# Performance work log

Hardware: AMD Instinct MI355X
Metric: run time of the kernel (lower is better)

The kernel has to match this reference:

```python
import jax, jax.numpy as jnp
import numpy as np


def setup_inputs() -> dict:
    key = jax.random.key(0)
    ks = jax.random.split(key, 6)
    B, T, D, H = 32, 2048, 1024, 1024
    s = jax.random.normal(ks[0], (1, B, D), dtype=jnp.float32)
    h = jax.random.normal(ks[1], (B, T, D), dtype=jnp.float32)
    mask = jax.random.randint(ks[2], (B, T), 0, 2, dtype=jnp.int32)
    W = jax.random.normal(ks[3], (D, H), dtype=jnp.float32) * (6.0 / (D + H)) ** 0.5
    U = jax.random.normal(ks[4], (D, H), dtype=jnp.float32) * (6.0 / (D + H)) ** 0.5
    v = jax.random.normal(ks[5], (H, 1), dtype=jnp.float32) * (6.0 / (H + 1)) ** 0.5
    return {"s": s, "h": h, "mask": mask, "W": W, "U": U, "v": v}


def reference(s, h, mask, W, U, v):
    # mask-fill encoder states: zero out padded timesteps
    m = (mask != 0)[:, :, None]            # (B, T, 1)
    h = jnp.where(m, h, 0.0)               # (B, T, D)
    s_t = jnp.transpose(s, (1, 0, 2))      # (B, 1, D)
    proj_s = s_t @ W                       # (B, 1, H)
    proj_h = h @ U                         # (B, T, H)
    energy = jnp.tanh(proj_s + proj_h) @ v  # (B, T, 1)
    energy = jnp.where(m, energy, -1e9)
    score = jax.nn.softmax(energy, axis=1)  # softmax over time
    context = jnp.sum(score * h, axis=1)    # (B, D)
    return context
```

## Files before the change

### kernel.cpp

```cpp
#include <hip/hip_runtime.h>
#include <hip/hip_fp16.h>
#include <math.h>

#define BB 32
#define TT 2048
#define DD 1024
#define HH 1024
#define MM (BB*TT)

typedef _Float16 half8 __attribute__((ext_vector_type(8)));
typedef float f32x4 __attribute__((ext_vector_type(4)));

__device__ __forceinline__ float tanh_fast(float x) {
    float cx = fminf(fmaxf(x, -10.0f), 10.0f);
    float e2 = __expf(2.0f * cx);
    return (e2 - 1.0f) / (e2 + 1.0f);
}

__device__ __forceinline__ void load_lds16(const _Float16* g, _Float16* l) {
    __builtin_amdgcn_global_load_lds(
        (const __attribute__((address_space(1))) void*)g,
        (__attribute__((address_space(3))) void*)l, 16, 0, 0);
}

__global__ void compact_kernel(const int* __restrict__ mask,
                               int* __restrict__ rowlist,
                               int* __restrict__ cnts) {
    const int b = blockIdx.x, tid = threadIdx.x;
    const int lane = tid & 63, w = tid >> 6;
    const int* mb = mask + b * TT;
    const int t0 = tid * 8;
    int m[8], c = 0;
#pragma unroll
    for (int j = 0; j < 8; ++j) { m[j] = (mb[t0 + j] != 0); c += m[j]; }
    int pref = c;
#pragma unroll
    for (int off = 1; off < 64; off <<= 1) {
        int nv = __shfl_up(pref, off, 64);
        if (lane >= off) pref += nv;
    }
    __shared__ int wsum[4];
    if (lane == 63) wsum[w] = pref;
    __syncthreads();
    int wbase = 0;
    for (int i = 0; i < w; ++i) wbase += wsum[i];
    int pos = wbase + pref - c;
#pragma unroll
    for (int j = 0; j < 8; ++j)
        if (m[j]) rowlist[b * TT + pos++] = t0 + j;
    const int total = wsum[0] + wsum[1] + wsum[2] + wsum[3];
    if (tid == 0) cnts[b] = total;
    __syncthreads();
    const int padded = ((total + 127) >> 7) << 7;
    const int lastt = (total > 0) ? rowlist[b * TT + total - 1] : 0;
    for (int ci = total + tid; ci < padded; ci += 256)
        rowlist[b * TT + ci] = lastt;
}

__global__ void tiles_kernel(const int* __restrict__ cnts,
                             int* __restrict__ tile_b,
                             int* __restrict__ tile_ci,
                             int* __restrict__ ntiles) {
    if (threadIdx.x == 0) {
        int tot = 0;
        for (int b = 0; b < BB; ++b) {
            const int nt = (cnts[b] + 127) >> 7;
            for (int i = 0; i < nt; ++i) { tile_b[tot] = b; tile_ci[tot] = i * 128; ++tot; }
        }
        *ntiles = tot;
    }
}

__global__ void cast_h_kernel(const float* __restrict__ h,
                              const int* __restrict__ mask,
                              _Float16* __restrict__ h16) {
    const int row = blockIdx.x * 2 + (threadIdx.x >> 7);
    if (mask[row] == 0) return;
    const int c = (threadIdx.x & 127) * 8;
    const long base = (long)row * DD + c;
    const float4 f0 = *(const float4*)(h + base);
    const float4 f1 = *(const float4*)(h + base + 4);
    half8 o;
    o[0] = (_Float16)f0.x; o[1] = (_Float16)f0.y;
    o[2] = (_Float16)f0.z; o[3] = (_Float16)f0.w;
    o[4] = (_Float16)f1.x; o[5] = (_Float16)f1.y;
    o[6] = (_Float16)f1.z; o[7] = (_Float16)f1.w;
    *(half8*)(h16 + base) = o;
}

__global__ void prep_ut_kernel(const float* __restrict__ U,
                               _Float16* __restrict__ Ut) {
    __shared__ float tile[32][33];
    const int bx = blockIdx.x, by = blockIdx.y;
    const int tx = threadIdx.x & 31, ty = threadIdx.x >> 5;
#pragma unroll
    for (int j = 0; j < 4; ++j)
        tile[ty + j * 8][tx] = U[(long)(by * 32 + ty + j * 8) * HH + bx * 32 + tx];
    __syncthreads();
#pragma unroll
    for (int j = 0; j < 4; ++j)
        Ut[(long)(bx * 32 + ty + j * 8) * DD + by * 32 + tx] =
            (_Float16)tile[tx][ty + j * 8];
}

__global__ void prep_ps_kernel(const float* __restrict__ s,
                               const float* __restrict__ W,
                               float* __restrict__ ps,
                               float* __restrict__ out) {
    const int b = blockIdx.x, nseg = blockIdx.y;
    const int n = nseg * 256 + threadIdx.x;
    __shared__ float ss[DD];
#pragma unroll
    for (int j = 0; j < 4; ++j)
        ss[threadIdx.x + j * 256] = s[b * DD + threadIdx.x + j * 256];
    out[b * DD + n] = 0.0f;
    __syncthreads();
    float a[8];
#pragma unroll
    for (int j = 0; j < 8; ++j) a[j] = 0.f;
    for (int d = 0; d < DD; d += 8) {
#pragma unroll
        for (int j = 0; j < 8; ++j)
            a[j] += ss[d + j] * W[(long)(d + j) * HH + n];
    }
    ps[b * HH + n] = ((a[0]+a[1])+(a[2]+a[3])) + ((a[4]+a[5])+(a[6]+a[7]));
}

#define Bb_K 32

__global__ __launch_bounds__(256)
void energy_gemm_kernel(const _Float16* __restrict__ h16,
                        const _Float16* __restrict__ Ut,
                        const float* __restrict__ ps,
                        const float* __restrict__ v,
                        const int* __restrict__ rowlist,
                        const int* __restrict__ tile_b,
                        const int* __restrict__ tile_ci,
                        const int* __restrict__ ntiles,
                        float* __restrict__ epart) {
    const int mt = blockIdx.y;
    if (mt >= *ntiles) return;
    __shared__ _Float16 As[128][32];
    __shared__ _Float16 Bs[128][32];
    __shared__ float ps_s[128];
    __shared__ float v_s[128];
    __shared__ int   rl[128];

    const int nt = blockIdx.x;
    const int b   = tile_b[mt];
    const int ci0 = tile_ci[mt];
    const int n0  = nt * 128;
    const int tid = threadIdx.x;
    const int wave = tid >> 6, lane = tid & 63;
    const int wm = wave >> 1, wn = wave & 1;

    if (tid < 128) {
        ps_s[tid] = ps[b * HH + n0 + tid];
        v_s[tid]  = v[n0 + tid];
        rl[tid]   = rowlist[b * TT + ci0 + tid];
    }
    __syncthreads();

    const int srow = wave * 32 + (lane >> 2);
    const int sseg = (lane & 3) * 8;
    const _Float16* gA0 = h16 + ((long)b * TT + rl[srow])      * DD + sseg;
    const _Float16* gA1 = h16 + ((long)b * TT + rl[srow + 16]) * DD + sseg;
    const _Float16* gB0 = Ut + (long)(n0 + srow) * DD + sseg;
    const _Float16* gB1 = gB0 + 16 * DD;
    _Float16* lA0 = &As[wave * 32][0];
    _Float16* lA1 = &As[wave * 32 + 16][0];
    _Float16* lB0 = &Bs[wave * 32][0];
    _Float16* lB1 = &Bs[wave * 32 + 16][0];

    f32x4 acc[4][4];
#pragma unroll
    for (int i = 0; i < 4; ++i)
#pragma unroll
        for (int j = 0; j < 4; ++j) acc[i][j] = (f32x4)0.0f;

    const int lk = (lane >> 4) * 8;
    const int lr = lane & 15;

#pragma unroll 1
    for (int k0 = 0; k0 < DD; k0 += Bb_K) {
        __syncthreads();
        load_lds16(gA0 + k0, lA0);
        load_lds16(gA1 + k0, lA1);
        load_lds16(gB0 + k0, lB0);
        load_lds16(gB1 + k0, lB1);
        __syncthreads();

        half8 af[4], bf[4];
#pragma unroll
        for (int tm = 0; tm < 4; ++tm)
            af[tm] = *(const half8*)&As[wm * 64 + tm * 16 + lr][lk];
#pragma unroll
        for (int tn = 0; tn < 4; ++tn)
            bf[tn] = *(const half8*)&Bs[wn * 64 + tn * 16 + lr][lk];
#pragma unroll
        for (int tm = 0; tm < 4; ++tm)
#pragma unroll
            for (int tn = 0; tn < 4; ++tn)
                acc[tm][tn] = __builtin_amdgcn_mfma_f32_16x16x32_f16(
                    af[tm], bf[tn], acc[tm][tn], 0, 0, 0);
    }

    float part[4][4];
#pragma unroll
    for (int tm = 0; tm < 4; ++tm) {
#pragma unroll
        for (int r = 0; r < 4; ++r) {
            float p = 0.f;
#pragma unroll
            for (int tn = 0; tn < 4; ++tn) {
                const int cl = wn * 64 + tn * 16 + lr;
                p += v_s[cl] * tanh_fast(acc[tm][tn][r] + ps_s[cl]);
            }
            part[tm][r] = p;
        }
    }
#pragma unroll
    for (int off = 1; off < 16; off <<= 1)
#pragma unroll
        for (int tm = 0; tm < 4; ++tm)
#pragma unroll
            for (int r = 0; r < 4; ++r)
                part[tm][r] += __shfl_xor(part[tm][r], off, 64);

    if ((lane & 15) == 0) {
        const int slot = nt * 2 + wn;
#pragma unroll
        for (int tm = 0; tm < 4; ++tm)
#pragma unroll
            for (int r = 0; r < 4; ++r) {
                const int ci = ci0 + wm * 64 + tm * 16 + (lane >> 4) * 4 + r;
                epart[(long)slot * MM + b * TT + ci] = part[tm][r];
            }
    }
}

__global__ void softmax_kernel(const float* __restrict__ epart,
                               const int* __restrict__ rowlist,
                               const int* __restrict__ cnts,
                               float* __restrict__ score) {
    const int b = blockIdx.x, tid = threadIdx.x;
    const int cnt = cnts[b];
    for (int t = tid; t < TT; t += 256) score[b * TT + t] = 0.0f;

    float e[8], mx = -1e30f;
#pragma unroll
    for (int i = 0; i < 8; ++i) {
        const int ci = i * 256 + tid;
        float sum = -1e30f;
        if (ci < cnt) {
            sum = 0.f;
#pragma unroll
            for (int p = 0; p < 16; ++p)
                sum += epart[(long)p * MM + b * TT + ci];
        }
        e[i] = sum;
        mx = fmaxf(mx, sum);
    }
#pragma unroll
    for (int off = 32; off > 0; off >>= 1) mx = fmaxf(mx, __shfl_xor(mx, off, 64));
    __shared__ float r4[4];
    if ((tid & 63) == 0) r4[tid >> 6] = mx;
    __syncthreads();
    mx = fmaxf(fmaxf(r4[0], r4[1]), fmaxf(r4[2], r4[3]));

    float tot = 0.f;
#pragma unroll
    for (int i = 0; i < 8; ++i) {
        const int ci = i * 256 + tid;
        e[i] = (ci < cnt) ? __expf(e[i] - mx) : 0.0f;
        tot += e[i];
    }
#pragma unroll
    for (int off = 32; off > 0; off >>= 1) tot += __shfl_xor(tot, off, 64);
    __shared__ float s4[4];
    if ((tid & 63) == 0) s4[tid >> 6] = tot;
    __syncthreads();
    tot = s4[0] + s4[1] + s4[2] + s4[3];
    const float inv = 1.0f / tot;
#pragma unroll
    for (int i = 0; i < 8; ++i) {
        const int ci = i * 256 + tid;
        if (ci < cnt)
            score[b * TT + rowlist[b * TT + ci]] = e[i] * inv;
    }
}

__global__ void context_kernel(const _Float16* __restrict__ h16,
                               const float* __restrict__ score,
                               float* __restrict__ out) {
    const int tc = blockIdx.x;
    const int b  = blockIdx.y;
    const int d0 = threadIdx.x * 8;
    float a[8];
#pragma unroll
    for (int j = 0; j < 8; ++j) a[j] = 0.f;
    for (int i = 0; i < 128; ++i) {
        const int t = tc * 128 + i;
        const float sc = score[(long)b * TT + t];
        if (sc != 0.0f) {
            const half8 hv = *(const half8*)(h16 + ((long)(b * TT + t)) * DD + d0);
#pragma unroll
            for (int j = 0; j < 8; ++j) a[j] += sc * (float)hv[j];
        }
    }
#pragma unroll
    for (int j = 0; j < 8; ++j) atomicAdd(&out[b * DD + d0 + j], a[j]);
}

extern "C" void kernel_launch(void* const* d_in, const int* in_sizes, int n_in,
                              void* d_out, int out_size, void* d_ws, size_t ws_size,
                              hipStream_t stream) {
    const float* s    = (const float*)d_in[0];
    const float* h    = (const float*)d_in[1];
    const int*   mask = (const int*)  d_in[2];
    const float* W    = (const float*)d_in[3];
    const float* U    = (const float*)d_in[4];
    const float* v    = (const float*)d_in[5];
    float* out = (float*)d_out;

    char* ws = (char*)d_ws;
    size_t off = 0;
    _Float16* h16 = (_Float16*)(ws + off); off += (size_t)MM * DD * 2;
    _Float16* Ut  = (_Float16*)(ws + off); off += (size_t)HH * DD * 2;
    float*    ps  = (float*)(ws + off);    off += (size_t)BB * HH * 4;
    float*    ep  = (float*)(ws + off);    off += (size_t)16 * MM * 4;
    float*    scr = (float*)(ws + off);    off += (size_t)MM * 4;
    int*      rlist = (int*)(ws + off);    off += (size_t)MM * 4;
    int*      cnts  = (int*)(ws + off);    off += 64 * 4;
    int*      tb    = (int*)(ws + off);    off += 512 * 4;
    int*      tci   = (int*)(ws + off);    off += 512 * 4;
    int*      ntl   = (int*)(ws + off);

    compact_kernel<<<BB, 256, 0, stream>>>(mask, rlist, cnts);
    tiles_kernel  <<<1, 64, 0, stream>>>(cnts, tb, tci, ntl);
    cast_h_kernel <<<MM / 2, 256, 0, stream>>>(h, mask, h16);
    prep_ut_kernel<<<dim3(32, 32), 256, 0, stream>>>(U, Ut);
    prep_ps_kernel<<<dim3(32, 4), 256, 0, stream>>>(s, W, ps, out);
    energy_gemm_kernel<<<dim3(8, 512), 256, 0, stream>>>(h16, Ut, ps, v,
                                                         rlist, tb, tci, ntl, ep);
    softmax_kernel<<<BB, 256, 0, stream>>>(ep, rlist, cnts, scr);
    context_kernel<<<dim3(16, 32), 128, 0, stream>>>(h16, scr, out);
}
```

Before: 559.7 us.

## Fuse setup kernels, drop tile list, swizzle LDS and raise MFMA priority

Merges the compaction, cast, U transpose and s·W projection kernels into one launch that dispatches on block index. The separate tile-list kernel goes away: each GEMM block derives its batch and row chunk from its index and exits early when past the valid count. The grid is reordered so the M-tile is the fast dimension, an XOR swizzle is applied to the LDS k-segment to reduce bank conflicts on fragment reads, and s_setprio is raised around the MFMA block. The GEMM now launches a fixed 512x8 grid with early-exit blocks, and the fused setup kernel shares one LDS allocation across its roles.

```diff
diff --git a/kernel.cpp b/kernel.cpp
--- a/kernel.cpp
+++ b/kernel.cpp
@@ -23,107 +23,113 @@
         (__attribute__((address_space(3))) void*)l, 16, 0, 0);
 }
 
-__global__ void compact_kernel(const int* __restrict__ mask,
-                               int* __restrict__ rowlist,
-                               int* __restrict__ cnts) {
-    const int b = blockIdx.x, tid = threadIdx.x;
-    const int lane = tid & 63, w = tid >> 6;
-    const int* mb = mask + b * TT;
-    const int t0 = tid * 8;
-    int m[8], c = 0;
-#pragma unroll
-    for (int j = 0; j < 8; ++j) { m[j] = (mb[t0 + j] != 0); c += m[j]; }
-    int pref = c;
-#pragma unroll
-    for (int off = 1; off < 64; off <<= 1) {
-        int nv = __shfl_up(pref, off, 64);
-        if (lane >= off) pref += nv;
-    }
+#define CAST_BLOCKS (MM/2)
+#define UT_BLOCKS   1024
+#define PS_BLOCKS   128
+#define CPT_BLOCKS  32
+#define TOTAL_SETUP (CAST_BLOCKS + UT_BLOCKS + PS_BLOCKS + CPT_BLOCKS)
+
+__global__ __launch_bounds__(256)
+void mega_setup_kernel(const float* __restrict__ h,
+                       const int* __restrict__ mask,
+                       _Float16* __restrict__ h16,
+                       const float* __restrict__ U,
+                       _Float16* __restrict__ Ut,
+                       const float* __restrict__ s,
+                       const float* __restrict__ W,
+                       float* __restrict__ ps,
+                       float* __restrict__ out,
+                       int* __restrict__ rowlist,
+                       int* __restrict__ cnts) {
+    __shared__ float smem[1056];
     __shared__ int wsum[4];
-    if (lane == 63) wsum[w] = pref;
-    __syncthreads();
-    int wbase = 0;
-    for (int i = 0; i < w; ++i) wbase += wsum[i];
-    int pos = wbase + pref - c;
-#pragma unroll
-    for (int j = 0; j < 8; ++j)
-        if (m[j]) rowlist[b * TT + pos++] = t0 + j;
-    const int total = wsum[0] + wsum[1] + wsum[2] + wsum[3];
-    if (tid == 0) cnts[b] = total;
-    __syncthreads();
-    const int padded = ((total + 127) >> 7) << 7;
-    const int lastt = (total > 0) ? rowlist[b * TT + total - 1] : 0;
-    for (int ci = total + tid; ci < padded; ci += 256)
-        rowlist[b * TT + ci] = lastt;
-}
-
-__global__ void tiles_kernel(const int* __restrict__ cnts,
-                             int* __restrict__ tile_b,
-                             int* __restrict__ tile_ci,
-                             int* __restrict__ ntiles) {
-    if (threadIdx.x == 0) {
-        int tot = 0;
-        for (int b = 0; b < BB; ++b) {
-            const int nt = (cnts[b] + 127) >> 7;
-            for (int i = 0; i < nt; ++i) { tile_b[tot] = b; tile_ci[tot] = i * 128; ++tot; }
-        }
-        *ntiles = tot;
-    }
-}
-
-__global__ void cast_h_kernel(const float* __restrict__ h,
-                              const int* __restrict__ mask,
-                              _Float16* __restrict__ h16) {
-    const int row = blockIdx.x * 2 + (threadIdx.x >> 7);
-    if (mask[row] == 0) return;
-    const int c = (threadIdx.x & 127) * 8;
-    const long base = (long)row * DD + c;
-    const float4 f0 = *(const float4*)(h + base);
-    const float4 f1 = *(const float4*)(h + base + 4);
-    half8 o;
-    o[0] = (_Float16)f0.x; o[1] = (_Float16)f0.y;
-    o[2] = (_Float16)f0.z; o[3] = (_Float16)f0.w;
-    o[4] = (_Float16)f1.x; o[5] = (_Float16)f1.y;
-    o[6] = (_Float16)f1.z; o[7] = (_Float16)f1.w;
-    *(half8*)(h16 + base) = o;
-}
-
-__global__ void prep_ut_kernel(const float* __restrict__ U,
-                               _Float16* __restrict__ Ut) {
-    __shared__ float tile[32][33];
-    const int bx = blockIdx.x, by = blockIdx.y;
-    const int tx = threadIdx.x & 31, ty = threadIdx.x >> 5;
-#pragma unroll
-    for (int j = 0; j < 4; ++j)
-        tile[ty + j * 8][tx] = U[(long)(by * 32 + ty + j * 8) * HH + bx * 32 + tx];
-    __syncthreads();
-#pragma unroll
-    for (int j = 0; j < 4; ++j)
-        Ut[(long)(bx * 32 + ty + j * 8) * DD + by * 32 + tx] =
-            (_Float16)tile[tx][ty + j * 8];
-}
-
-__global__ void prep_ps_kernel(const float* __restrict__ s,
-                               const float* __restrict__ W,
-                               float* __restrict__ ps,
-                               float* __restrict__ out) {
-    const int b = blockIdx.x, nseg = blockIdx.y;
-    const int n = nseg * 256 + threadIdx.x;
-    __shared__ float ss[DD];
-#pragma unroll
-    for (int j = 0; j < 4; ++j)
-        ss[threadIdx.x + j * 256] = s[b * DD + threadIdx.x + j * 256];
-    out[b * DD + n] = 0.0f;
-    __syncthreads();
-    float a[8];
-#pragma unroll
-    for (int j = 0; j < 8; ++j) a[j] = 0.f;
-    for (int d = 0; d < DD; d += 8) {
+    const int bid = blockIdx.x;
+    const int tid = threadIdx.x;
+
+    if (bid < CAST_BLOCKS) {
+        const int row = bid * 2 + (tid >> 7);
+        if (mask[row] == 0) return;
+        const int c = (tid & 127) * 8;
+        const long base = (long)row * DD + c;
+        const float4 f0 = *(const float4*)(h + base);
+        const float4 f1 = *(const float4*)(h + base + 4);
+        half8 o;
+        o[0] = (_Float16)f0.x; o[1] = (_Float16)f0.y;
+        o[2] = (_Float16)f0.z; o[3] = (_Float16)f0.w;
+        o[4] = (_Float16)f1.x; o[5] = (_Float16)f1.y;
+        o[6] = (_Float16)f1.z; o[7] = (_Float16)f1.w;
+        *(half8*)(h16 + base) = o;
+        return;
+    }
+
+    if (bid < CAST_BLOCKS + UT_BLOCKS) {
+        const int id = bid - CAST_BLOCKS;
+        const int bx = id & 31, by = id >> 5;
+        float (*tile)[33] = (float(*)[33])smem;
+        const int tx = tid & 31, ty = tid >> 5;
+#pragma unroll
+        for (int j = 0; j < 4; ++j)
+            tile[ty + j * 8][tx] = U[(long)(by * 32 + ty + j * 8) * HH + bx * 32 + tx];
+        __syncthreads();
+#pragma unroll
+        for (int j = 0; j < 4; ++j)
+            Ut[(long)(bx * 32 + ty + j * 8) * DD + by * 32 + tx] =
+                (_Float16)tile[tx][ty + j * 8];
+        return;
+    }
+
+    if (bid < CAST_BLOCKS + UT_BLOCKS + PS_BLOCKS) {
+        const int id = bid - (CAST_BLOCKS + UT_BLOCKS);
+        const int b = id & 31, nseg = id >> 5;
+        const int n = nseg * 256 + tid;
+        float* ss = smem;
+#pragma unroll
+        for (int j = 0; j < 4; ++j)
+            ss[tid + j * 256] = s[b * DD + tid + j * 256];
+        out[b * DD + n] = 0.0f;
+        __syncthreads();
+        float a[8];
+#pragma unroll
+        for (int j = 0; j < 8; ++j) a[j] = 0.f;
+        for (int d = 0; d < DD; d += 8) {
+#pragma unroll
+            for (int j = 0; j < 8; ++j)
+                a[j] += ss[d + j] * W[(long)(d + j) * HH + n];
+        }
+        ps[b * HH + n] = ((a[0]+a[1])+(a[2]+a[3])) + ((a[4]+a[5])+(a[6]+a[7]));
+        return;
+    }
+
+    {
+        const int b = bid - (CAST_BLOCKS + UT_BLOCKS + PS_BLOCKS);
+        const int lane = tid & 63, w = tid >> 6;
+        const int* mb = mask + b * TT;
+        const int t0 = tid * 8;
+        int m[8], c = 0;
+#pragma unroll
+        for (int j = 0; j < 8; ++j) { m[j] = (mb[t0 + j] != 0); c += m[j]; }
+        int pref = c;
+#pragma unroll
+        for (int off = 1; off < 64; off <<= 1) {
+            int nv = __shfl_up(pref, off, 64);
+            if (lane >= off) pref += nv;
+        }
+        if (lane == 63) wsum[w] = pref;
+        __syncthreads();
+        int wbase = 0;
+        for (int i = 0; i < w; ++i) wbase += wsum[i];
+        int pos = wbase + pref - c;
 #pragma unroll
         for (int j = 0; j < 8; ++j)
-            a[j] += ss[d + j] * W[(long)(d + j) * HH + n];
-    }
-    ps[b * HH + n] = ((a[0]+a[1])+(a[2]+a[3])) + ((a[4]+a[5])+(a[6]+a[7]));
+            if (m[j]) rowlist[b * TT + pos++] = t0 + j;
+        const int total = wsum[0] + wsum[1] + wsum[2] + wsum[3];
+        if (tid == 0) cnts[b] = total;
+        __syncthreads();
+        const int padded = ((total + 127) >> 7) << 7;
+        const int lastt = (total > 0) ? rowlist[b * TT + total - 1] : 0;
+        for (int ci = total + tid; ci < padded; ci += 256)
+            rowlist[b * TT + ci] = lastt;
+    }
 }
 
 #define Bb_K 32
@@ -134,21 +140,20 @@
                         const float* __restrict__ ps,
                         const float* __restrict__ v,
                         const int* __restrict__ rowlist,
-                        const int* __restrict__ tile_b,
-                        const int* __restrict__ tile_ci,
-                        const int* __restrict__ ntiles,
+                        const int* __restrict__ cnts,
                         float* __restrict__ epart) {
-    const int mt = blockIdx.y;
-    if (mt >= *ntiles) return;
+    const int mt = blockIdx.x;
+    const int nt = blockIdx.y;
+    const int b   = mt >> 4;
+    const int ci0 = (mt & 15) << 7;
+    if (ci0 >= cnts[b]) return;
+
     __shared__ _Float16 As[128][32];
     __shared__ _Float16 Bs[128][32];
     __shared__ float ps_s[128];
     __shared__ float v_s[128];
     __shared__ int   rl[128];
 
-    const int nt = blockIdx.x;
-    const int b   = tile_b[mt];
-    const int ci0 = tile_ci[mt];
     const int n0  = nt * 128;
     const int tid = threadIdx.x;
     const int wave = tid >> 6, lane = tid & 63;
@@ -162,7 +167,7 @@
     __syncthreads();
 
     const int srow = wave * 32 + (lane >> 2);
-    const int sseg = (lane & 3) * 8;
+    const int sseg = ((lane & 3) ^ ((lane >> 2) & 3)) * 8;
     const _Float16* gA0 = h16 + ((long)b * TT + rl[srow])      * DD + sseg;
     const _Float16* gA1 = h16 + ((long)b * TT + rl[srow + 16]) * DD + sseg;
     const _Float16* gB0 = Ut + (long)(n0 + srow) * DD + sseg;
@@ -178,8 +183,8 @@
 #pragma unroll
         for (int j = 0; j < 4; ++j) acc[i][j] = (f32x4)0.0f;
 
-    const int lk = (lane >> 4) * 8;
     const int lr = lane & 15;
+    const int lk = (((lane >> 4) ^ (lr & 3))) * 8;
 
 #pragma unroll 1
     for (int k0 = 0; k0 < DD; k0 += Bb_K) {
@@ -197,12 +202,14 @@
 #pragma unroll
         for (int tn = 0; tn < 4; ++tn)
             bf[tn] = *(const half8*)&Bs[wn * 64 + tn * 16 + lr][lk];
+        __builtin_amdgcn_s_setprio(1);
 #pragma unroll
         for (int tm = 0; tm < 4; ++tm)
 #pragma unroll
             for (int tn = 0; tn < 4; ++tn)
                 acc[tm][tn] = __builtin_amdgcn_mfma_f32_16x16x32_f16(
                     af[tm], bf[tn], acc[tm][tn], 0, 0, 0);
+        __builtin_amdgcn_s_setprio(0);
     }
 
     float part[4][4];
@@ -332,17 +339,11 @@
     float*    scr = (float*)(ws + off);    off += (size_t)MM * 4;
     int*      rlist = (int*)(ws + off);    off += (size_t)MM * 4;
     int*      cnts  = (int*)(ws + off);    off += 64 * 4;
-    int*      tb    = (int*)(ws + off);    off += 512 * 4;
-    int*      tci   = (int*)(ws + off);    off += 512 * 4;
-    int*      ntl   = (int*)(ws + off);
-
-    compact_kernel<<<BB, 256, 0, stream>>>(mask, rlist, cnts);
-    tiles_kernel  <<<1, 64, 0, stream>>>(cnts, tb, tci, ntl);
-    cast_h_kernel <<<MM / 2, 256, 0, stream>>>(h, mask, h16);
-    prep_ut_kernel<<<dim3(32, 32), 256, 0, stream>>>(U, Ut);
-    prep_ps_kernel<<<dim3(32, 4), 256, 0, stream>>>(s, W, ps, out);
-    energy_gemm_kernel<<<dim3(8, 512), 256, 0, stream>>>(h16, Ut, ps, v,
-                                                         rlist, tb, tci, ntl, ep);
+
+    mega_setup_kernel<<<TOTAL_SETUP, 256, 0, stream>>>(h, mask, h16, U, Ut,
+                                                       s, W, ps, out, rlist, cnts);
+    energy_gemm_kernel<<<dim3(512, 8), 256, 0, stream>>>(h16, Ut, ps, v,
+                                                         rlist, cnts, ep);
     softmax_kernel<<<BB, 256, 0, stream>>>(ep, rlist, cnts, scr);
     context_kernel<<<dim3(16, 32), 128, 0, stream>>>(h16, scr, out);
 }
```

After: 616.8 us. 10.2% more time.
